# Kernel optimization log

Hardware: AMD Instinct MI355X
Metric: run time of the kernel (lower is better)

## Reference

```python
import jax, jax.numpy as jnp
import numpy as np

B, S, E, H, DH = 4, 2048, 2048, 16, 256  # DH = mlp hidden (d_hid)
HD = E // H  # per-head dim = 128
EPS = 1e-5

def _ln(x, w, b):
    m = jnp.mean(x, axis=-1, keepdims=True)
    v = jnp.mean(jnp.square(x - m), axis=-1, keepdims=True)
    return (x - m) * jax.lax.rsqrt(v + EPS) * w + b

def setup_inputs() -> dict:
    key = jax.random.key(0)
    ks = jax.random.split(key, 10)
    s = 0.02
    return {
        "x": jax.random.normal(ks[0], (B, S, E), jnp.float32),
        "attention_mask": jax.random.randint(ks[1], (B, S), 0, 2, jnp.int32),
        "ln1_w": jnp.ones((E,), jnp.float32),
        "ln1_b": jnp.zeros((E,), jnp.float32),
        "in_proj_w": jax.random.normal(ks[2], (3 * E, E), jnp.float32) * s,
        "in_proj_b": jnp.zeros((3 * E,), jnp.float32),
        "out_proj_w": jax.random.normal(ks[3], (E, E), jnp.float32) * s,
        "out_proj_b": jnp.zeros((E,), jnp.float32),
        "ln2_w": jnp.ones((E,), jnp.float32),
        "ln2_b": jnp.zeros((E,), jnp.float32),
        "mlp_w1": jax.random.normal(ks[4], (DH, E), jnp.float32) * s,
        "mlp_b1": jnp.zeros((DH,), jnp.float32),
        "mlp_w2": jax.random.normal(ks[5], (E, DH), jnp.float32) * s,
        "mlp_b2": jnp.zeros((E,), jnp.float32),
    }

def reference(x, attention_mask, ln1_w, ln1_b, in_proj_w, in_proj_b,
              out_proj_w, out_proj_b, ln2_w, ln2_b, mlp_w1, mlp_b1, mlp_w2, mlp_b2):
    h = _ln(x, ln1_w, ln1_b)
    qkv = h @ in_proj_w.T + in_proj_b  # [B,S,3E]
    q, k, v = jnp.split(qkv, 3, axis=-1)
    q = q.reshape(B, S, H, HD).transpose(0, 2, 1, 3) / jnp.sqrt(jnp.float32(HD))
    k = k.reshape(B, S, H, HD).transpose(0, 2, 1, 3)
    v = v.reshape(B, S, H, HD).transpose(0, 2, 1, 3)
    scores = jnp.einsum("bhqd,bhkd->bhqk", q, k)
    # Faithful to source: FLOAT attn_mask of +1.0 on strictly-upper triangle (additive),
    # NOT -inf; key_padding_mask positions do get -inf.
    causal_add = jnp.triu(jnp.ones((S, S), jnp.float32), k=1)
    scores = scores + causal_add
    pad = (attention_mask == 0)  # True = padded key
    scores = jnp.where(pad[:, None, None, :], jnp.float32(-jnp.inf), scores)
    attn = jax.nn.softmax(scores, axis=-1)
    ctx = jnp.einsum("bhqk,bhkd->bhqd", attn, v)
    ctx = ctx.transpose(0, 2, 1, 3).reshape(B, S, E)
    x = x + ctx @ out_proj_w.T + out_proj_b
    h2 = _ln(x, ln2_w, ln2_b)
    mlp = jax.nn.relu(h2 @ mlp_w1.T + mlp_b1) @ mlp_w2.T + mlp_b2
    return x + mlp
```

## Files before the change

kernel.cpp:

```cpp
#include <hip/hip_runtime.h>

typedef __attribute__((ext_vector_type(8))) short short8;
typedef __attribute__((ext_vector_type(4))) float f32x4;
typedef __attribute__((ext_vector_type(16))) float f32x16;

typedef __attribute__((address_space(1))) const void gas1_t;
typedef __attribute__((address_space(3))) void las3_t;
#define GLL16(g, l) __builtin_amdgcn_global_load_lds((gas1_t*)(g), (las3_t*)(l), 16, 0, 0)

__device__ inline unsigned short f2bf(float f) {
  union { float f; unsigned int u; } v; v.f = f;
  unsigned int r = v.u + 0x7FFFu + ((v.u >> 16) & 1u);
  return (unsigned short)(r >> 16);
}

__device__ inline float exp2_fast(float x) {
  float r; asm("v_exp_f32 %0, %1" : "=v"(r) : "v"(x)); return r;
}

__global__ __launch_bounds__(256) void ln_kernel(const float* __restrict__ x,
                                                 const float* __restrict__ w,
                                                 const float* __restrict__ bia,
                                                 unsigned short* __restrict__ out) {
  const int row = blockIdx.x;
  const int tid = threadIdx.x;
  const float* xr = x + (size_t)row * 2048;
  float4 a = *(const float4*)(xr + tid * 8);
  float4 b = *(const float4*)(xr + tid * 8 + 4);
  float s  = a.x + a.y + a.z + a.w + b.x + b.y + b.z + b.w;
  float s2 = a.x*a.x + a.y*a.y + a.z*a.z + a.w*a.w + b.x*b.x + b.y*b.y + b.z*b.z + b.w*b.w;
  #pragma unroll
  for (int off = 1; off < 64; off <<= 1) {
    s  += __shfl_xor(s, off);
    s2 += __shfl_xor(s2, off);
  }
  __shared__ float red[8];
  if ((tid & 63) == 0) { red[tid >> 6] = s; red[4 + (tid >> 6)] = s2; }
  __syncthreads();
  s  = red[0] + red[1] + red[2] + red[3];
  s2 = red[4] + red[5] + red[6] + red[7];
  const float mean = s * (1.f / 2048.f);
  const float var  = s2 * (1.f / 2048.f) - mean * mean;
  const float rstd = rsqrtf(var + 1e-5f);
  float4 wa = *(const float4*)(w + tid * 8), wb = *(const float4*)(w + tid * 8 + 4);
  float4 ba = *(const float4*)(bia + tid * 8), bb = *(const float4*)(bia + tid * 8 + 4);
  short8 o;
  o[0] = (short)f2bf((a.x - mean) * rstd * wa.x + ba.x);
  o[1] = (short)f2bf((a.y - mean) * rstd * wa.y + ba.y);
  o[2] = (short)f2bf((a.z - mean) * rstd * wa.z + ba.z);
  o[3] = (short)f2bf((a.w - mean) * rstd * wa.w + ba.w);
  o[4] = (short)f2bf((b.x - mean) * rstd * wb.x + bb.x);
  o[5] = (short)f2bf((b.y - mean) * rstd * wb.y + bb.y);
  o[6] = (short)f2bf((b.z - mean) * rstd * wb.z + bb.z);
  o[7] = (short)f2bf((b.w - mean) * rstd * wb.w + bb.w);
  *(short8*)(out + (size_t)row * 2048 + tid * 8) = o;
}

__global__ __launch_bounds__(256) void conv_kernel(const float* __restrict__ in,
                                                   unsigned short* __restrict__ out, int n) {
  size_t idx = ((size_t)blockIdx.x * 256 + threadIdx.x) * 8;
  if (idx >= (size_t)n) return;
  float4 a = *(const float4*)(in + idx);
  float4 b = *(const float4*)(in + idx + 4);
  short8 o;
  o[0] = (short)f2bf(a.x); o[1] = (short)f2bf(a.y);
  o[2] = (short)f2bf(a.z); o[3] = (short)f2bf(a.w);
  o[4] = (short)f2bf(b.x); o[5] = (short)f2bf(b.y);
  o[6] = (short)f2bf(b.z); o[7] = (short)f2bf(b.w);
  *(short8*)(out + idx) = o;
}

template <int MODE>
__global__ __launch_bounds__(256) void gemm_bt(const unsigned short* __restrict__ A,
                                               const unsigned short* __restrict__ Bw,
                                               const float* __restrict__ bias,
                                               const float* __restrict__ res,
                                               void* __restrict__ outp,
                                               void* __restrict__ outp2,
                                               int M, int N, int K) {
  __shared__ unsigned short As[128 * 64];
  __shared__ unsigned short Bs[128 * 64];
  const int tid = threadIdx.x;
  const int l = tid & 63, wv = tid >> 6;
  const int l15 = l & 15, l4 = l >> 4;
  const int wr = wv >> 1, wc = wv & 1;
  const int nx = gridDim.x;
  const int nwg = nx * gridDim.y;
  const int bidlin = blockIdx.y * nx + blockIdx.x;
  const int cpx = nwg >> 3;
  const int swz = (bidlin & 7) * cpx + (bidlin >> 3);
  const int m0 = (swz / nx) * 128, n0 = (swz % nx) * 128;

  f32x4 acc[4][4] = {};
  for (int k0 = 0; k0 < K; k0 += 64) {
    __syncthreads();
    #pragma unroll
    for (int i = 0; i < 4; ++i) {
      int e = i * 2048 + tid * 8;
      int r = e >> 6;
      int c = (e ^ ((r & 7) << 3)) & 63;
      GLL16(A + (size_t)(m0 + r) * K + k0 + c, As + e);
      GLL16(Bw + (size_t)(n0 + r) * K + k0 + c, Bs + e);
    }
    __syncthreads();
    #pragma unroll
    for (int kk = 0; kk < 64; kk += 32) {
      short8 af[4], bfr[4];
      #pragma unroll
      for (int m = 0; m < 4; ++m) {
        int r = wr * 64 + m * 16 + l15;
        int byt = (r * 128 + (kk + l4 * 8) * 2) ^ ((r & 7) << 4);
        af[m] = *(const short8*)((const char*)As + byt);
      }
      #pragma unroll
      for (int n = 0; n < 4; ++n) {
        int r = wc * 64 + n * 16 + l15;
        int byt = (r * 128 + (kk + l4 * 8) * 2) ^ ((r & 7) << 4);
        bfr[n] = *(const short8*)((const char*)Bs + byt);
      }
      #pragma unroll
      for (int m = 0; m < 4; ++m)
        #pragma unroll
        for (int n = 0; n < 4; ++n)
          acc[m][n] = __builtin_amdgcn_mfma_f32_16x16x32_bf16(af[m], bfr[n], acc[m][n], 0, 0, 0);
    }
  }
  #pragma unroll
  for (int m = 0; m < 4; ++m) {
    #pragma unroll
    for (int n = 0; n < 4; ++n) {
      #pragma unroll
      for (int r = 0; r < 4; ++r) {
        int row = m0 + wr * 64 + m * 16 + l4 * 4 + r;
        int col = n0 + wc * 64 + n * 16 + l15;
        float v = acc[m][n][r] + bias[col];
        if (MODE == 0) {
          unsigned short val = f2bf(v);
          if (col < 4096) ((unsigned short*)outp)[(size_t)row * 4096 + col] = val;
          else            ((unsigned short*)outp2)[(size_t)row * 2048 + col - 4096] = val;
        } else if (MODE == 1) {
          ((unsigned short*)outp)[(size_t)row * N + col] = f2bf(v > 0.f ? v : 0.f);
        } else {
          ((float*)outp)[(size_t)row * N + col] = res[(size_t)row * N + col] + v;
        }
      }
    }
  }
}

__global__ __launch_bounds__(256) void vtrans_kernel(const unsigned short* __restrict__ v,
                                                     unsigned short* __restrict__ vT) {
  __shared__ unsigned short T[128 * 128];
  const int t0 = blockIdx.x * 128;
  const int b = blockIdx.y >> 4, h = blockIdx.y & 15;
  const int tid = threadIdx.x;
  const int tl = tid >> 4, l16 = tid & 15, c8 = l16 * 8;
  #pragma unroll
  for (int i = 0; i < 8; ++i) {
    int t = tl + i * 16;
    short8 val = *(const short8*)(v + (size_t)(b * 2048 + t0 + t) * 2048 + h * 128 + c8);
    *(short8*)((char*)T + ((t * 256 + c8 * 2) ^ ((t & 7) << 4))) = val;
  }
  __syncthreads();
  #pragma unroll
  for (int i = 0; i < 8; ++i) {
    int d = tl + i * 16;
    unsigned short* orow = vT + ((size_t)(b * 16 + h) * 128 + d) * 2048 + t0;
    #pragma unroll
    for (int j = 0; j < 8; ++j) {
      int t = l16 + 16 * j;
      orow[t] = *(const unsigned short*)((const char*)T + ((t * 256 + d * 2) ^ ((t & 7) << 4)));
    }
  }
}

__global__ __launch_bounds__(256) void attn_kernel(const unsigned short* __restrict__ qk,
                                                   const unsigned short* __restrict__ vT,
                                                   const int* __restrict__ amask,
                                                   unsigned short* __restrict__ ctx) {
  __shared__ unsigned short Ks[2][4096];
  __shared__ unsigned short Vs[2][4096];
  __shared__ unsigned short Pl[4][1152];

  const int qt = blockIdx.x, bh = blockIdx.y;
  const int b = bh >> 4, h = bh & 15;
  const int tid = threadIdx.x;
  const int wv = tid >> 6, l = tid & 63;
  const int l31 = l & 31, hi = l >> 5;
  const int q0w = qt * 128 + wv * 32;
  const float SC2 = 0.08838834764831845f * 1.4426950408889634f;
  const float L2E = 1.4426950408889634f;
  const float MF  = 10.0f;

  int kinv[2], vinv[2];
  #pragma unroll
  for (int c = 0; c < 2; ++c) {
    int e = c * 2048 + tid * 8;
    int key = e >> 7, d0 = e & 127;
    kinv[c] = key * 4096 + 2048 + h * 128 + (d0 ^ ((key & 7) << 3));
    int d = e >> 5, kchunk = ((e >> 3) & 3) ^ ((d & 6) >> 1);
    vinv[c] = d * 2048 + kchunk * 8;
  }
  const unsigned short* kb0 = qk + (size_t)(b * 2048) * 4096;
  const unsigned short* vb0 = vT + (size_t)(b * 16 + h) * (128 * 2048);
  const int* mrow = amask + b * 2048;

  short8 qf[8];
  {
    const unsigned short* qp = qk + (size_t)(b * 2048 + q0w + l31) * 4096 + h * 128 + hi * 8;
    #pragma unroll
    for (int c = 0; c < 8; ++c) qf[c] = *(const short8*)(qp + c * 16);
  }

  short8 vones;
  #pragma unroll
  for (int j = 0; j < 8; ++j) vones[j] = (short)0x3F80;

  f32x16 o[4] = {};
  f32x16 ol = {};

  #pragma unroll
  for (int c = 0; c < 2; ++c) {
    GLL16(kb0 + kinv[c], &Ks[0][c * 2048 + tid * 8]);
    GLL16(vb0 + vinv[c], &Vs[0][c * 2048 + tid * 8]);
  }
  __syncthreads();

  for (int kt = 0; kt < 2048; kt += 32) {
    const int cur = (kt >> 5) & 1;
    if (kt + 32 < 2048) {
      #pragma unroll
      for (int c = 0; c < 2; ++c) {
        GLL16(kb0 + (size_t)(kt + 32) * 4096 + kinv[c], &Ks[cur ^ 1][c * 2048 + tid * 8]);
        GLL16(vb0 + (kt + 32) + vinv[c], &Vs[cur ^ 1][c * 2048 + tid * 8]);
      }
    }
    const bool pad = (mrow[kt + l31] == 0);

    f32x16 sacc = {};
    __builtin_amdgcn_s_setprio(1);
    #pragma unroll
    for (int c = 0; c < 8; ++c) {
      short8 kf = *(const short8*)((const char*)Ks[cur] +
                   ((l31 * 256 + c * 32 + hi * 16) ^ ((l31 & 7) << 4)));
      sacc = __builtin_amdgcn_mfma_f32_32x32x16_bf16(qf[c], kf, sacc, 0, 0, 0);
    }
    __builtin_amdgcn_s_setprio(0);

    float s[16];
    if (kt > q0w + 31) {
      #pragma unroll
      for (int i = 0; i < 16; ++i) s[i] = sacc[i] * SC2 + L2E;
    } else if (kt + 31 <= q0w) {
      #pragma unroll
      for (int i = 0; i < 16; ++i) s[i] = sacc[i] * SC2;
    } else {
      int kg = kt + l31;
      #pragma unroll
      for (int i = 0; i < 16; ++i) {
        int qg = q0w + (i & 3) + 8 * (i >> 2) + 4 * hi;
        s[i] = sacc[i] * SC2 + ((kg > qg) ? L2E : 0.f);
      }
    }
    if (pad) {
      #pragma unroll
      for (int i = 0; i < 16; ++i) s[i] = -1e30f;
    }

    #pragma unroll
    for (int i = 0; i < 16; ++i) {
      int q = (i & 3) + 8 * (i >> 2) + 4 * hi;
      Pl[wv][q * 36 + l31] = f2bf(exp2_fast(s[i] - MF));
    }
    short8 pa0 = *(const short8*)&Pl[wv][l31 * 36 + hi * 8];
    short8 pa1 = *(const short8*)&Pl[wv][l31 * 36 + 16 + hi * 8];

    __builtin_amdgcn_s_setprio(1);
    #pragma unroll
    for (int g = 0; g < 4; ++g) {
      int d = g * 32 + l31;
      int swzd = (d & 6) << 3;
      short8 vf0 = *(const short8*)((const char*)Vs[cur] + ((d * 64 + hi * 16) ^ swzd));
      o[g] = __builtin_amdgcn_mfma_f32_32x32x16_bf16(pa0, vf0, o[g], 0, 0, 0);
      short8 vf1 = *(const short8*)((const char*)Vs[cur] + ((d * 64 + 32 + hi * 16) ^ swzd));
      o[g] = __builtin_amdgcn_mfma_f32_32x32x16_bf16(pa1, vf1, o[g], 0, 0, 0);
    }
    ol = __builtin_amdgcn_mfma_f32_32x32x16_bf16(pa0, vones, ol, 0, 0, 0);
    ol = __builtin_amdgcn_mfma_f32_32x32x16_bf16(pa1, vones, ol, 0, 0, 0);
    __builtin_amdgcn_s_setprio(0);

    __syncthreads();
  }

  float inv[16];
  #pragma unroll
  for (int i = 0; i < 16; ++i) inv[i] = 1.0f / ol[i];
  #pragma unroll
  for (int g = 0; g < 4; ++g) {
    #pragma unroll
    for (int i = 0; i < 16; ++i) {
      int q = q0w + (i & 3) + 8 * (i >> 2) + 4 * hi;
      ctx[(size_t)(b * 2048 + q) * 2048 + h * 128 + g * 32 + l31] = f2bf(o[g][i] * inv[i]);
    }
  }
}

extern "C" void kernel_launch(void* const* d_in, const int* in_sizes, int n_in,
                              void* d_out, int out_size, void* d_ws, size_t ws_size,
                              hipStream_t stream) {
  (void)in_sizes; (void)n_in; (void)out_size; (void)ws_size;
  const float* x    = (const float*)d_in[0];
  const int*   am   = (const int*)d_in[1];
  const float* ln1w = (const float*)d_in[2];
  const float* ln1b = (const float*)d_in[3];
  const float* win  = (const float*)d_in[4];
  const float* bin  = (const float*)d_in[5];
  const float* wout = (const float*)d_in[6];
  const float* bout = (const float*)d_in[7];
  const float* ln2w = (const float*)d_in[8];
  const float* ln2b = (const float*)d_in[9];
  const float* w1   = (const float*)d_in[10];
  const float* b1   = (const float*)d_in[11];
  const float* w2   = (const float*)d_in[12];
  const float* b2   = (const float*)d_in[13];
  float* out = (float*)d_out;

  char* ws = (char*)d_ws;
  unsigned short* hbuf = (unsigned short*)ws;
  unsigned short* vTb  = (unsigned short*)ws;
  unsigned short* qkb  = (unsigned short*)(ws + (size_t)32 * 1048576);
  unsigned short* h2b  = (unsigned short*)(ws + (size_t)32 * 1048576);
  unsigned short* midb = (unsigned short*)(ws + (size_t)64 * 1048576);
  unsigned short* vbuf = (unsigned short*)(ws + (size_t)96 * 1048576);
  unsigned short* ctxb = (unsigned short*)(ws + (size_t)96 * 1048576);
  unsigned short* wbuf = (unsigned short*)(ws + (size_t)128 * 1048576);

  ln_kernel<<<dim3(8192), dim3(256), 0, stream>>>(x, ln1w, ln1b, hbuf);
  conv_kernel<<<dim3(6144), dim3(256), 0, stream>>>(win, wbuf, 12582912);
  gemm_bt<0><<<dim3(48, 64), dim3(256), 0, stream>>>(hbuf, wbuf, bin, (const float*)nullptr,
                                                     (void*)qkb, (void*)vbuf, 8192, 6144, 2048);
  vtrans_kernel<<<dim3(16, 64), dim3(256), 0, stream>>>(vbuf, vTb);
  attn_kernel<<<dim3(16, 64), dim3(256), 0, stream>>>(qkb, vTb, am, ctxb);
  conv_kernel<<<dim3(2048), dim3(256), 0, stream>>>(wout, wbuf, 4194304);
  gemm_bt<2><<<dim3(16, 64), dim3(256), 0, stream>>>(ctxb, wbuf, bout, x,
                                                     (void*)out, nullptr, 8192, 2048, 2048);
  ln_kernel<<<dim3(8192), dim3(256), 0, stream>>>(out, ln2w, ln2b, h2b);
  conv_kernel<<<dim3(256), dim3(256), 0, stream>>>(w1, wbuf, 524288);
  gemm_bt<1><<<dim3(2, 64), dim3(256), 0, stream>>>(h2b, wbuf, b1, (const float*)nullptr,
                                                    (void*)midb, nullptr, 8192, 256, 2048);
  conv_kernel<<<dim3(256), dim3(256), 0, stream>>>(w2, wbuf, 524288);
  gemm_bt<2><<<dim3(16, 64), dim3(256), 0, stream>>>(midb, wbuf, b2, out,
                                                     (void*)out, nullptr, 8192, 2048, 256);
}
```

Before: 704.5 us.

## Add 256x256-tile 8-wave pipelined GEMM for QKV and out-projection

Adds a new gemm8 kernel that uses 256x256 output tiles with 512 threads. It stages operands with global_load_lds into double-buffered, XOR-swizzled LDS, interleaves loads with MFMA phases under explicit vmcnt waits and priority hints, and swizzles block order for L2 locality. The large QKV and out-projection GEMMs now use it, while the MLP GEMMs keep the old kernel. The larger tiles should raise operand reuse and hide memory latency, at the cost of more LDS and registers per block and fragile hand-tuned waitcnt scheduling.

After: 655.2 us. 7.0% less time.

```diff
diff --git a/kernel.cpp b/kernel.cpp
--- a/kernel.cpp
+++ b/kernel.cpp
@@ -16,6 +16,12 @@
 
 __device__ inline float exp2_fast(float x) {
   float r; asm("v_exp_f32 %0, %1" : "=v"(r) : "v"(x)); return r;
+}
+
+__device__ inline void vmwait(int n) {
+  if (n == 6)      asm volatile("s_waitcnt vmcnt(6)" ::: "memory");
+  else if (n == 4) asm volatile("s_waitcnt vmcnt(4)" ::: "memory");
+  else             asm volatile("s_waitcnt vmcnt(0)" ::: "memory");
 }
 
 __global__ __launch_bounds__(256) void ln_kernel(const float* __restrict__ x,
@@ -134,12 +140,114 @@
         int row = m0 + wr * 64 + m * 16 + l4 * 4 + r;
         int col = n0 + wc * 64 + n * 16 + l15;
         float v = acc[m][n][r] + bias[col];
+        if (MODE == 1) {
+          ((unsigned short*)outp)[(size_t)row * N + col] = f2bf(v > 0.f ? v : 0.f);
+        } else {
+          ((float*)outp)[(size_t)row * N + col] = res[(size_t)row * N + col] + v;
+        }
+      }
+    }
+  }
+}
+
+template <int MODE>
+__global__ __launch_bounds__(512, 2) void gemm8(const unsigned short* __restrict__ A,
+                                                const unsigned short* __restrict__ Bw,
+                                                const float* __restrict__ bias,
+                                                const float* __restrict__ res,
+                                                void* __restrict__ outp,
+                                                void* __restrict__ outp2,
+                                                int M, int N, int K) {
+  __shared__ char LA[2][2][16384];
+  __shared__ char LB[2][2][16384];
+  const int tid = threadIdx.x;
+  const int l = tid & 63, wv = tid >> 6;
+  const int l15 = l & 15, l4 = l >> 4;
+  const int wr = wv >> 2, wc = wv & 3;
+  const int nx = gridDim.x;
+  const int nwg = nx * gridDim.y;
+  const int bidlin = blockIdx.y * nx + blockIdx.x;
+  const int cpx = nwg >> 3;
+  const int swz = (bidlin & 7) * cpx + (bidlin >> 3);
+  const int m0 = (swz / nx) * 256, n0 = (swz % nx) * 256;
+
+  int srow0, scol0, srow1, scol1;
+  {
+    int o = tid * 16, p = o >> 7, i = o & 127;
+    srow0 = 2 * p + ((i >> 6) & 1);
+    scol0 = (((i >> 4) & 3) ^ (p & 3)) * 8;
+    o = 8192 + tid * 16; p = o >> 7; i = o & 127;
+    srow1 = 2 * p + ((i >> 6) & 1);
+    scol1 = (((i >> 4) & 3) ^ (p & 3)) * 8;
+  }
+
+#define STG_A(t, kh) { int kk = (t) * 64 + (kh) * 32; \
+    GLL16(A + (size_t)(m0 + srow0) * K + kk + scol0, &LA[(t) & 1][kh][tid * 16]); \
+    GLL16(A + (size_t)(m0 + srow1) * K + kk + scol1, &LA[(t) & 1][kh][8192 + tid * 16]); }
+#define STG_B(t, kh) { int kk = (t) * 64 + (kh) * 32; \
+    GLL16(Bw + (size_t)(n0 + srow0) * K + kk + scol0, &LB[(t) & 1][kh][tid * 16]); \
+    GLL16(Bw + (size_t)(n0 + srow1) * K + kk + scol1, &LB[(t) & 1][kh][8192 + tid * 16]); }
+
+#define LDSOFF(r, c4) (((r) >> 1) * 128 + (((((r) & 1) << 6) + ((c4) << 4)) ^ ((((r) >> 1) & 3) << 4)))
+
+  f32x4 acc[8][4] = {};
+  const int NT = K >> 6, iters = NT >> 1;
+
+  STG_A(0, 0); STG_B(0, 0); STG_A(0, 1); STG_B(0, 1); STG_A(1, 0);
+  vmwait(6);
+  __builtin_amdgcn_s_barrier();
+
+#define PH(t, kh, mh, STG, VM) { \
+    short8 af[4], bf[4]; \
+    const char* Ab = LA[(t) & 1][kh]; \
+    const char* Bb = LB[(t) & 1][kh]; \
+    _Pragma("unroll") for (int f = 0; f < 4; ++f) { \
+      int ra = wr * 128 + ((mh) * 4 + f) * 16 + l15; \
+      af[f] = *(const short8*)(Ab + LDSOFF(ra, l4)); \
+      int rb = wc * 64 + f * 16 + l15; \
+      bf[f] = *(const short8*)(Bb + LDSOFF(rb, l4)); } \
+    STG; \
+    __builtin_amdgcn_s_barrier(); \
+    asm volatile("s_waitcnt lgkmcnt(0)" ::: "memory"); \
+    __builtin_amdgcn_sched_barrier(0); \
+    __builtin_amdgcn_s_setprio(1); \
+    _Pragma("unroll") for (int f = 0; f < 4; ++f) \
+      _Pragma("unroll") for (int n = 0; n < 4; ++n) \
+        acc[(mh) * 4 + f][n] = __builtin_amdgcn_mfma_f32_16x16x32_bf16(af[f], bf[n], acc[(mh) * 4 + f][n], 0, 0, 0); \
+    __builtin_amdgcn_s_setprio(0); \
+    if ((VM) >= 0) vmwait(VM); \
+    __builtin_amdgcn_s_barrier(); }
+
+  for (int i = 0; i < iters; ++i) {
+    const int T0 = 2 * i, T1 = 2 * i + 1, T2 = 2 * i + 2, T3 = 2 * i + 3;
+    const bool last = (i == iters - 1);
+    PH(T0, 0, 0, STG_B(T1, 0), -1);
+    PH(T0, 0, 1, STG_A(T1, 1), 6);
+    PH(T0, 1, 0, STG_B(T1, 1), -1);
+    PH(T0, 1, 1, if (T2 < NT) STG_A(T2, 0), last ? 4 : 6);
+    PH(T1, 0, 0, if (T2 < NT) STG_B(T2, 0), -1);
+    PH(T1, 0, 1, if (T2 < NT) STG_A(T2, 1), last ? 0 : 6);
+    PH(T1, 1, 0, if (T2 < NT) STG_B(T2, 1), -1);
+    PH(T1, 1, 1, if (T3 < NT) STG_A(T3, 0), last ? -1 : 6);
+  }
+#undef PH
+#undef STG_A
+#undef STG_B
+#undef LDSOFF
+
+  #pragma unroll
+  for (int mf = 0; mf < 8; ++mf) {
+    #pragma unroll
+    for (int nf = 0; nf < 4; ++nf) {
+      #pragma unroll
+      for (int r = 0; r < 4; ++r) {
+        int row = m0 + wr * 128 + mf * 16 + l4 * 4 + r;
+        int col = n0 + wc * 64 + nf * 16 + l15;
+        float v = acc[mf][nf][r] + bias[col];
         if (MODE == 0) {
           unsigned short val = f2bf(v);
           if (col < 4096) ((unsigned short*)outp)[(size_t)row * 4096 + col] = val;
           else            ((unsigned short*)outp2)[(size_t)row * 2048 + col - 4096] = val;
-        } else if (MODE == 1) {
-          ((unsigned short*)outp)[(size_t)row * N + col] = f2bf(v > 0.f ? v : 0.f);
         } else {
           ((float*)outp)[(size_t)row * N + col] = res[(size_t)row * N + col] + v;
         }
@@ -337,13 +445,13 @@
 
   ln_kernel<<<dim3(8192), dim3(256), 0, stream>>>(x, ln1w, ln1b, hbuf);
   conv_kernel<<<dim3(6144), dim3(256), 0, stream>>>(win, wbuf, 12582912);
-  gemm_bt<0><<<dim3(48, 64), dim3(256), 0, stream>>>(hbuf, wbuf, bin, (const float*)nullptr,
-                                                     (void*)qkb, (void*)vbuf, 8192, 6144, 2048);
+  gemm8<0><<<dim3(24, 32), dim3(512), 0, stream>>>(hbuf, wbuf, bin, (const float*)nullptr,
+                                                   (void*)qkb, (void*)vbuf, 8192, 6144, 2048);
   vtrans_kernel<<<dim3(16, 64), dim3(256), 0, stream>>>(vbuf, vTb);
   attn_kernel<<<dim3(16, 64), dim3(256), 0, stream>>>(qkb, vTb, am, ctxb);
   conv_kernel<<<dim3(2048), dim3(256), 0, stream>>>(wout, wbuf, 4194304);
-  gemm_bt<2><<<dim3(16, 64), dim3(256), 0, stream>>>(ctxb, wbuf, bout, x,
-                                                     (void*)out, nullptr, 8192, 2048, 2048);
+  gemm8<2><<<dim3(8, 32), dim3(512), 0, stream>>>(ctxb, wbuf, bout, x,
+                                                  (void*)out, nullptr, 8192, 2048, 2048);
   ln_kernel<<<dim3(8192), dim3(256), 0, stream>>>(out, ln2w, ln2b, h2b);
   conv_kernel<<<dim3(256), dim3(256), 0, stream>>>(w1, wbuf, 524288);
   gemm_bt<1><<<dim3(2, 64), dim3(256), 0, stream>>>(h2b, wbuf, b1, (const float*)nullptr,
```
